# Kernel optimization log

Hardware: AMD Instinct MI355X
Metric: run time of the kernel (lower is better)

## Reference

```python
import jax, jax.numpy as jnp
import numpy as np

BN_EPS = 1e-3  # O-CNN default bn_eps
N_NODES = 150000
C_IN, C_OUT, K = 32, 64, 27  # 3x3x3 octree stencil


def setup_inputs() -> dict:
    key = jax.random.key(0)
    k1, k2, k3 = jax.random.split(key, 3)
    data_in = jax.random.normal(k1, (1, C_IN, N_NODES, 1), dtype=jnp.float32)
    # neighbor table: index == N_NODES marks an empty (zero) neighbor
    neigh = jax.random.randint(k2, (N_NODES, K), 0, N_NODES + 1, dtype=jnp.int32)
    W = jax.random.normal(k3, (C_OUT, C_IN, K), dtype=jnp.float32) * 0.05
    gamma = jnp.ones((C_OUT,), dtype=jnp.float32)
    beta = jnp.zeros((C_OUT,), dtype=jnp.float32)
    return {"data_in": data_in, "neigh": neigh, "W": W, "gamma": gamma, "beta": beta}


def reference(data_in, neigh, W, gamma, beta):
    # data_in: [1, C_in, N, 1] (O-CNN octree feature layout)
    x = data_in[0, :, :, 0]                                  # [C_in, N]
    # pad one zero column so neighbor index == N gathers zeros (empty octant)
    x_pad = jnp.concatenate([x, jnp.zeros((x.shape[0], 1), x.dtype)], axis=1)
    g = x_pad[:, neigh]                                      # [C_in, N, K] im2col gather
    y = jnp.einsum('oik,ink->on', W, g)                      # [C_out, N] GEMM
    # BatchNorm2d (training mode): stats per channel over all nodes, biased var
    mean = jnp.mean(y, axis=1, keepdims=True)
    var = jnp.mean(jnp.square(y - mean), axis=1, keepdims=True)
    yn = (y - mean) * jax.lax.rsqrt(var + BN_EPS)
    out = jnp.maximum(yn * gamma[:, None] + beta[:, None], 0.0)  # affine + ReLU
    return out[None, :, :, None]                             # [1, C_out, N, 1]
```

## Files before the change

kernel.cpp:

```cpp
#include <hip/hip_runtime.h>
#include <hip/hip_bf16.h>
#include <stdint.h>

#define N_NODES 150000
#define C_IN 32
#define C_OUT 64
#define K_TAPS 27
#define K_PAD 28
#define PF 3
#define NSTEP 7
#define NSLOTS 32
#define Y_STRIDE 150016

#define TRANS_BLOCKS 2344
#define WPREP_BLOCKS 224
#define CONV_BLOCKS 4688
#define WS_NEED 28934656ull

typedef __attribute__((ext_vector_type(8))) __bf16 bf16x8;
typedef __attribute__((ext_vector_type(4))) float f32x4;
typedef __attribute__((ext_vector_type(4))) uint32_t u32x4;

__device__ __forceinline__ ushort f2bf(float f) {
    union { float f; uint32_t u; } v; v.f = f;
    uint32_t u = v.u;
    return (ushort)((u + 0x7FFFu + ((u >> 16) & 1u)) >> 16);
}

__global__ __launch_bounds__(256) void k_prep(const float* __restrict__ x,
                                              ushort* __restrict__ xT,
                                              const float* __restrict__ W,
                                              ushort* __restrict__ A_frag,
                                              float* __restrict__ stats) {
    int t = threadIdx.x;
    int b = blockIdx.x;
    if (b < TRANS_BLOCKS) {
        __shared__ float tile[32][65];
        int nb = b * 64;
        int nl = t & 63, i4 = t >> 6;
#pragma unroll
        for (int rep = 0; rep < 8; ++rep) {
            int i = rep * 4 + i4;
            int n = nb + nl;
            tile[i][nl] = (n < N_NODES) ? x[(size_t)i * N_NODES + n] : 0.0f;
        }
        __syncthreads();
        int nr = t >> 2, c0 = (t & 3) * 8;
        int n = nb + nr;
        if (n <= N_NODES) {
            uint32_t w[4];
#pragma unroll
            for (int j = 0; j < 4; ++j) {
                ushort lo = f2bf(tile[c0 + 2 * j][nr]);
                ushort hi = f2bf(tile[c0 + 2 * j + 1][nr]);
                w[j] = (uint32_t)lo | ((uint32_t)hi << 16);
            }
            *reinterpret_cast<uint4*>(xT + (size_t)n * 32 + c0) =
                make_uint4(w[0], w[1], w[2], w[3]);
        }
    } else {
        int tid = (b - TRANS_BLOCKS) * 256 + t;
        if (tid < NSLOTS * 128 + 128) stats[tid] = 0.0f;
        if (tid < C_OUT * C_IN * K_PAD) {
            int j = tid & 7;
            int ln = (tid >> 3) & 63;
            int km = tid >> 9;
            int m = km & 3;
            int k = km >> 2;
            int o = m * 16 + (ln & 15);
            int i = (ln >> 4) * 8 + j;
            A_frag[tid] =
                (k < K_TAPS) ? f2bf(W[o * (C_IN * K_TAPS) + i * K_TAPS + k]) : (ushort)0;
        }
    }
}

__global__ __launch_bounds__(256, 4) void k_conv(const ushort* __restrict__ xT,
                                                 const ushort* __restrict__ A_frag,
                                                 const int* __restrict__ neigh,
                                                 float* __restrict__ yf,
                                                 ushort* __restrict__ yb,
                                                 float* __restrict__ stats,
                                                 int use_bf16) {
    __shared__ int soff[32 * K_PAD];
    __shared__ float sacc[C_OUT * 32];
    int t = threadIdx.x;
    int nb = blockIdx.x * 32;
    for (int j = t; j < 32 * K_PAD; j += 256) {
        int n = j / K_PAD;
        int kk = j - n * K_PAD;
        int ng = nb + n;
        int idx = (kk < K_TAPS && ng < N_NODES) ? neigh[(size_t)ng * K_TAPS + kk]
                                                : N_NODES;
        soff[j] = idx << 6;
    }
    __syncthreads();

    int wid = t >> 6, lane = t & 63;
    int l15 = lane & 15, quad = lane >> 4;
    int qoff = quad << 4;

    const char* xTb = (const char*)xT;
    const char* aB = (const char*)A_frag + (size_t)lane * 16;

    f32x4 acc[4][2];
#pragma unroll
    for (int m = 0; m < 4; ++m)
#pragma unroll
        for (int g = 0; g < 2; ++g) acc[m][g] = (f32x4){0.f, 0.f, 0.f, 0.f};

    bf16x8 bb[PF][2], aa[PF][4];
#pragma unroll
    for (int s = 0; s < PF; ++s) {
        int k = wid + 4 * s;
#pragma unroll
        for (int g = 0; g < 2; ++g)
            bb[s][g] = *reinterpret_cast<const bf16x8*>(
                xTb + (uint32_t)soff[(g * 16 + l15) * K_PAD + k] + qoff);
#pragma unroll
        for (int m = 0; m < 4; ++m)
            aa[s][m] = *reinterpret_cast<const bf16x8*>(aB + ((size_t)(k * 4 + m) << 10));
    }

#pragma unroll
    for (int s = 0; s < NSTEP; ++s) {
        int cur = s % PF;
#pragma unroll
        for (int m = 0; m < 4; ++m)
#pragma unroll
            for (int g = 0; g < 2; ++g)
                acc[m][g] = __builtin_amdgcn_mfma_f32_16x16x32_bf16(
                    aa[cur][m], bb[cur][g], acc[m][g], 0, 0, 0);
        if (s < NSTEP - PF) {
            int kn = wid + 4 * (s + PF);
#pragma unroll
            for (int g = 0; g < 2; ++g)
                bb[cur][g] = *reinterpret_cast<const bf16x8*>(
                    xTb + (uint32_t)soff[(g * 16 + l15) * K_PAD + kn] + qoff);
#pragma unroll
            for (int m = 0; m < 4; ++m)
                aa[cur][m] = *reinterpret_cast<const bf16x8*>(
                    aB + ((size_t)(kn * 4 + m) << 10));
        }
    }

    if (wid == 0) {
#pragma unroll
        for (int m = 0; m < 4; ++m)
#pragma unroll
            for (int g = 0; g < 2; ++g)
#pragma unroll
                for (int r = 0; r < 4; ++r)
                    sacc[(m * 16 + quad * 4 + r) * 32 + g * 16 + l15] = acc[m][g][r];
    }
    __syncthreads();
#pragma unroll
    for (int w = 1; w < 4; ++w) {
        if (wid == w) {
#pragma unroll
            for (int m = 0; m < 4; ++m)
#pragma unroll
                for (int g = 0; g < 2; ++g)
#pragma unroll
                    for (int r = 0; r < 4; ++r)
                        sacc[(m * 16 + quad * 4 + r) * 32 + g * 16 + l15] +=
                            acc[m][g][r];
        }
        __syncthreads();
    }

    if (use_bf16) {
        int e0 = t * 8;
        int o = t >> 2;
        int n0 = (t & 3) * 8;
        uint32_t w[4];
#pragma unroll
        for (int j = 0; j < 4; ++j) {
            ushort lo = f2bf(sacc[e0 + 2 * j]);
            ushort hi = f2bf(sacc[e0 + 2 * j + 1]);
            w[j] = (uint32_t)lo | ((uint32_t)hi << 16);
        }
        u32x4 v = {w[0], w[1], w[2], w[3]};
        __builtin_nontemporal_store(
            v, reinterpret_cast<u32x4*>(yb + (size_t)o * Y_STRIDE + nb + n0));
    } else {
#pragma unroll
        for (int rep = 0; rep < 8; ++rep) {
            int idx = rep * 256 + t;
            int o = idx >> 5;
            int n = nb + (idx & 31);
            if (n < N_NODES)
                __builtin_nontemporal_store(sacc[idx], &yf[(size_t)o * N_NODES + n]);
        }
    }

    if (wid == 0) {
        int slot = blockIdx.x & (NSLOTS - 1);
#pragma unroll
        for (int m = 0; m < 4; ++m) {
#pragma unroll
            for (int r = 0; r < 4; ++r) {
                int o = m * 16 + quad * 4 + r;
                float s = 0.f, sq = 0.f;
#pragma unroll
                for (int g = 0; g < 2; ++g) {
                    float v = sacc[o * 32 + g * 16 + l15];
                    s += v;
                    sq += v * v;
                }
#pragma unroll
                for (int d = 1; d < 16; d <<= 1) {
                    s += __shfl_xor(s, d);
                    sq += __shfl_xor(sq, d);
                }
                if (l15 == 0) {
                    atomicAdd(&stats[slot * 128 + o], s);
                    atomicAdd(&stats[slot * 128 + 64 + o], sq);
                }
            }
        }
    }
}

__global__ __launch_bounds__(256) void k_bn_relu(const ushort* __restrict__ yb,
                                                 float* __restrict__ out,
                                                 const float* __restrict__ stats,
                                                 const float* __restrict__ gamma,
                                                 const float* __restrict__ beta,
                                                 int use_bf16) {
    __shared__ float s_sc, s_sh;
    int t = threadIdx.x;
    int o = blockIdx.y;
    if (t < 32) {
        float s = stats[t * 128 + o];
        float sq = stats[t * 128 + 64 + o];
#pragma unroll
        for (int d = 1; d < 32; d <<= 1) {
            s += __shfl_xor(s, d);
            sq += __shfl_xor(sq, d);
        }
        if (t == 0) {
            const float invN = 1.0f / (float)N_NODES;
            float mean = s * invN;
            float var = sq * invN - mean * mean;
            float rstd = rsqrtf(var + 1e-3f);
            float sc = gamma[o] * rstd;
            s_sc = sc;
            s_sh = beta[o] - mean * sc;
        }
    }
    __syncthreads();
    float sc = s_sc, sh = s_sh;
    if (use_bf16) {
        const u32x4* row = reinterpret_cast<const u32x4*>(yb + (size_t)o * Y_STRIDE);
        f32x4* orow = reinterpret_cast<f32x4*>(out + (size_t)o * N_NODES);
#pragma unroll
        for (int it = 0; it < 2; ++it) {
            int c = blockIdx.x * 512 + it * 256 + t;
            if (c < N_NODES / 8) {
                u32x4 v = __builtin_nontemporal_load(row + c);
                f32x4 f0, f1;
#pragma unroll
                for (int j = 0; j < 2; ++j) {
                    f0[2 * j] = __uint_as_float(v[j] << 16);
                    f0[2 * j + 1] = __uint_as_float(v[j] & 0xffff0000u);
                    f1[2 * j] = __uint_as_float(v[j + 2] << 16);
                    f1[2 * j + 1] = __uint_as_float(v[j + 2] & 0xffff0000u);
                }
#pragma unroll
                for (int j = 0; j < 4; ++j) {
                    f0[j] = fmaxf(fmaf(f0[j], sc, sh), 0.f);
                    f1[j] = fmaxf(fmaf(f1[j], sc, sh), 0.f);
                }
                __builtin_nontemporal_store(f0, orow + 2 * c);
                __builtin_nontemporal_store(f1, orow + 2 * c + 1);
            }
        }
    } else {
        float4* row = reinterpret_cast<float4*>(out + (size_t)o * N_NODES);
        int base = blockIdx.x * 1024 + t;
#pragma unroll
        for (int it = 0; it < 4; ++it) {
            int i = base + it * 256;
            if (i < N_NODES / 4) {
                float4 v = row[i];
                v.x = fmaxf(fmaf(v.x, sc, sh), 0.f);
                v.y = fmaxf(fmaf(v.y, sc, sh), 0.f);
                v.z = fmaxf(fmaf(v.z, sc, sh), 0.f);
                v.w = fmaxf(fmaf(v.w, sc, sh), 0.f);
                row[i] = v;
            }
        }
    }
}

extern "C" void kernel_launch(void* const* d_in, const int* in_sizes, int n_in,
                              void* d_out, int out_size, void* d_ws, size_t ws_size,
                              hipStream_t stream) {
    const float* data_in = (const float*)d_in[0];
    const int* neigh = (const int*)d_in[1];
    const float* W = (const float*)d_in[2];
    const float* gamma = (const float*)d_in[3];
    const float* beta = (const float*)d_in[4];
    float* out = (float*)d_out;

    char* ws = (char*)d_ws;
    ushort* xT = (ushort*)ws;
    ushort* A_frag = (ushort*)(ws + 9601024);
    float* stats = (float*)(ws + 9715712);
    ushort* yb = (ushort*)(ws + 9732608);

    int use_bf16 = (ws_size >= WS_NEED) ? 1 : 0;

    k_prep<<<TRANS_BLOCKS + WPREP_BLOCKS, 256, 0, stream>>>(data_in, xT, W, A_frag,
                                                            stats);
    k_conv<<<CONV_BLOCKS, 256, 0, stream>>>(xT, A_frag, neigh, out, yb, stats,
                                            use_bf16);
    k_bn_relu<<<dim3(37, C_OUT), 256, 0, stream>>>(yb, out, stats, gamma, beta,
                                                   use_bf16);
}
```

Before: 171.6 us.

## Fuse conv and BN+ReLU into one persistent kernel with a grid barrier

Replaces the separate conv and BN/ReLU kernels with one persistent kernel of 1024 blocks. Each block loops over node tiles doing the gather-GEMM and accumulating per-channel statistics, then waits at a software grid barrier (an atomic counter that k_prep zeroes). After the barrier every block reduces the stats and applies the BN affine plus ReLU in a grid-stride pass. This removes one kernel launch and the gap between the two stages. In exchange it adds a spin-wait barrier, serialises tiles within each block, and relies on all 1024 blocks being resident at once to avoid deadlock.

```diff
diff --git a/kernel.cpp b/kernel.cpp
--- a/kernel.cpp
+++ b/kernel.cpp
@@ -14,7 +14,10 @@
 
 #define TRANS_BLOCKS 2344
 #define WPREP_BLOCKS 224
-#define CONV_BLOCKS 4688
+#define N_TILES 4688
+#define FUSED_BLOCKS 1024
+#define CHUNKS_PER_ROW 18750
+#define TOTAL_CHUNKS (C_OUT * CHUNKS_PER_ROW)
 #define WS_NEED 28934656ull
 
 typedef __attribute__((ext_vector_type(8))) __bf16 bf16x8;
@@ -75,221 +78,225 @@
     }
 }
 
-__global__ __launch_bounds__(256, 4) void k_conv(const ushort* __restrict__ xT,
-                                                 const ushort* __restrict__ A_frag,
-                                                 const int* __restrict__ neigh,
-                                                 float* __restrict__ yf,
-                                                 ushort* __restrict__ yb,
-                                                 float* __restrict__ stats,
-                                                 int use_bf16) {
+__global__ __launch_bounds__(256, 4) void k_fused(
+    const ushort* __restrict__ xT, const ushort* __restrict__ A_frag,
+    const int* __restrict__ neigh, float* __restrict__ out,
+    ushort* __restrict__ yb, float* __restrict__ stats, int* __restrict__ barrier_ctr,
+    const float* __restrict__ gamma, const float* __restrict__ beta, int use_bf16) {
     __shared__ int soff[32 * K_PAD];
     __shared__ float sacc[C_OUT * 32];
+    __shared__ float s_sc[C_OUT], s_sh[C_OUT];
     int t = threadIdx.x;
-    int nb = blockIdx.x * 32;
-    for (int j = t; j < 32 * K_PAD; j += 256) {
-        int n = j / K_PAD;
-        int kk = j - n * K_PAD;
-        int ng = nb + n;
-        int idx = (kk < K_TAPS && ng < N_NODES) ? neigh[(size_t)ng * K_TAPS + kk]
-                                                : N_NODES;
-        soff[j] = idx << 6;
-    }
-    __syncthreads();
-
     int wid = t >> 6, lane = t & 63;
     int l15 = lane & 15, quad = lane >> 4;
     int qoff = quad << 4;
-
     const char* xTb = (const char*)xT;
     const char* aB = (const char*)A_frag + (size_t)lane * 16;
 
-    f32x4 acc[4][2];
-#pragma unroll
-    for (int m = 0; m < 4; ++m)
-#pragma unroll
-        for (int g = 0; g < 2; ++g) acc[m][g] = (f32x4){0.f, 0.f, 0.f, 0.f};
-
-    bf16x8 bb[PF][2], aa[PF][4];
-#pragma unroll
-    for (int s = 0; s < PF; ++s) {
-        int k = wid + 4 * s;
-#pragma unroll
-        for (int g = 0; g < 2; ++g)
-            bb[s][g] = *reinterpret_cast<const bf16x8*>(
-                xTb + (uint32_t)soff[(g * 16 + l15) * K_PAD + k] + qoff);
+    for (int tile = blockIdx.x; tile < N_TILES; tile += FUSED_BLOCKS) {
+        int nb = tile * 32;
+        __syncthreads();
+        for (int j = t; j < 32 * K_PAD; j += 256) {
+            int n = j / K_PAD;
+            int kk = j - n * K_PAD;
+            int ng = nb + n;
+            int idx = (kk < K_TAPS && ng < N_NODES) ? neigh[(size_t)ng * K_TAPS + kk]
+                                                    : N_NODES;
+            soff[j] = idx << 6;
+        }
+        __syncthreads();
+
+        f32x4 acc[4][2];
 #pragma unroll
         for (int m = 0; m < 4; ++m)
-            aa[s][m] = *reinterpret_cast<const bf16x8*>(aB + ((size_t)(k * 4 + m) << 10));
-    }
-
-#pragma unroll
-    for (int s = 0; s < NSTEP; ++s) {
-        int cur = s % PF;
-#pragma unroll
-        for (int m = 0; m < 4; ++m)
+#pragma unroll
+            for (int g = 0; g < 2; ++g) acc[m][g] = (f32x4){0.f, 0.f, 0.f, 0.f};
+
+        bf16x8 bb[PF][2], aa[PF][4];
+#pragma unroll
+        for (int s = 0; s < PF; ++s) {
+            int k = wid + 4 * s;
 #pragma unroll
             for (int g = 0; g < 2; ++g)
-                acc[m][g] = __builtin_amdgcn_mfma_f32_16x16x32_bf16(
-                    aa[cur][m], bb[cur][g], acc[m][g], 0, 0, 0);
-        if (s < NSTEP - PF) {
-            int kn = wid + 4 * (s + PF);
-#pragma unroll
-            for (int g = 0; g < 2; ++g)
-                bb[cur][g] = *reinterpret_cast<const bf16x8*>(
-                    xTb + (uint32_t)soff[(g * 16 + l15) * K_PAD + kn] + qoff);
+                bb[s][g] = *reinterpret_cast<const bf16x8*>(
+                    xTb + (uint32_t)soff[(g * 16 + l15) * K_PAD + k] + qoff);
 #pragma unroll
             for (int m = 0; m < 4; ++m)
-                aa[cur][m] = *reinterpret_cast<const bf16x8*>(
-                    aB + ((size_t)(kn * 4 + m) << 10));
-        }
-    }
-
-    if (wid == 0) {
-#pragma unroll
-        for (int m = 0; m < 4; ++m)
-#pragma unroll
-            for (int g = 0; g < 2; ++g)
-#pragma unroll
-                for (int r = 0; r < 4; ++r)
-                    sacc[(m * 16 + quad * 4 + r) * 32 + g * 16 + l15] = acc[m][g][r];
-    }
+                aa[s][m] =
+                    *reinterpret_cast<const bf16x8*>(aB + ((size_t)(k * 4 + m) << 10));
+        }
+
+#pragma unroll
+        for (int s = 0; s < NSTEP; ++s) {
+            int cur = s % PF;
+#pragma unroll
+            for (int m = 0; m < 4; ++m)
+#pragma unroll
+                for (int g = 0; g < 2; ++g)
+                    acc[m][g] = __builtin_amdgcn_mfma_f32_16x16x32_bf16(
+                        aa[cur][m], bb[cur][g], acc[m][g], 0, 0, 0);
+            if (s < NSTEP - PF) {
+                int kn = wid + 4 * (s + PF);
+#pragma unroll
+                for (int g = 0; g < 2; ++g)
+                    bb[cur][g] = *reinterpret_cast<const bf16x8*>(
+                        xTb + (uint32_t)soff[(g * 16 + l15) * K_PAD + kn] + qoff);
+#pragma unroll
+                for (int m = 0; m < 4; ++m)
+                    aa[cur][m] = *reinterpret_cast<const bf16x8*>(
+                        aB + ((size_t)(kn * 4 + m) << 10));
+            }
+        }
+
+        if (wid == 0) {
+#pragma unroll
+            for (int m = 0; m < 4; ++m)
+#pragma unroll
+                for (int g = 0; g < 2; ++g)
+#pragma unroll
+                    for (int r = 0; r < 4; ++r)
+                        sacc[(m * 16 + quad * 4 + r) * 32 + g * 16 + l15] =
+                            acc[m][g][r];
+        }
+        __syncthreads();
+#pragma unroll
+        for (int w = 1; w < 4; ++w) {
+            if (wid == w) {
+#pragma unroll
+                for (int m = 0; m < 4; ++m)
+#pragma unroll
+                    for (int g = 0; g < 2; ++g)
+#pragma unroll
+                        for (int r = 0; r < 4; ++r)
+                            sacc[(m * 16 + quad * 4 + r) * 32 + g * 16 + l15] +=
+                                acc[m][g][r];
+            }
+            __syncthreads();
+        }
+
+        if (use_bf16) {
+            int e0 = t * 8;
+            int o = t >> 2;
+            int n0 = (t & 3) * 8;
+            uint32_t w[4];
+#pragma unroll
+            for (int j = 0; j < 4; ++j) {
+                ushort lo = f2bf(sacc[e0 + 2 * j]);
+                ushort hi = f2bf(sacc[e0 + 2 * j + 1]);
+                w[j] = (uint32_t)lo | ((uint32_t)hi << 16);
+            }
+            u32x4 v = {w[0], w[1], w[2], w[3]};
+            __builtin_nontemporal_store(
+                v, reinterpret_cast<u32x4*>(yb + (size_t)o * Y_STRIDE + nb + n0));
+        } else {
+#pragma unroll
+            for (int rep = 0; rep < 8; ++rep) {
+                int idx = rep * 256 + t;
+                int o = idx >> 5;
+                int n = nb + (idx & 31);
+                if (n < N_NODES)
+                    __builtin_nontemporal_store(sacc[idx],
+                                                &out[(size_t)o * N_NODES + n]);
+            }
+        }
+
+        if (wid == 0) {
+            int slot = tile & (NSLOTS - 1);
+#pragma unroll
+            for (int m = 0; m < 4; ++m) {
+#pragma unroll
+                for (int r = 0; r < 4; ++r) {
+                    int o = m * 16 + quad * 4 + r;
+                    float s = 0.f, sq = 0.f;
+#pragma unroll
+                    for (int g = 0; g < 2; ++g) {
+                        float v = sacc[o * 32 + g * 16 + l15];
+                        s += v;
+                        sq += v * v;
+                    }
+#pragma unroll
+                    for (int d = 1; d < 16; d <<= 1) {
+                        s += __shfl_xor(s, d);
+                        sq += __shfl_xor(sq, d);
+                    }
+                    if (l15 == 0) {
+                        atomicAdd(&stats[slot * 128 + o], s);
+                        atomicAdd(&stats[slot * 128 + 64 + o], sq);
+                    }
+                }
+            }
+        }
+    }
+
+    __threadfence();
     __syncthreads();
-#pragma unroll
-    for (int w = 1; w < 4; ++w) {
-        if (wid == w) {
-#pragma unroll
-            for (int m = 0; m < 4; ++m)
-#pragma unroll
-                for (int g = 0; g < 2; ++g)
-#pragma unroll
-                    for (int r = 0; r < 4; ++r)
-                        sacc[(m * 16 + quad * 4 + r) * 32 + g * 16 + l15] +=
-                            acc[m][g][r];
-        }
-        __syncthreads();
-    }
+    if (t == 0) {
+        __hip_atomic_fetch_add(barrier_ctr, 1, __ATOMIC_ACQ_REL,
+                               __HIP_MEMORY_SCOPE_AGENT);
+        while (__hip_atomic_load(barrier_ctr, __ATOMIC_ACQUIRE,
+                                 __HIP_MEMORY_SCOPE_AGENT) < FUSED_BLOCKS) {
+            __builtin_amdgcn_s_sleep(8);
+        }
+    }
+    __syncthreads();
+    __threadfence();
+
+    if (t < C_OUT) {
+        float s = 0.f, sq = 0.f;
+        for (int c = 0; c < NSLOTS; ++c) {
+            s += __hip_atomic_load(&stats[c * 128 + t], __ATOMIC_RELAXED,
+                                   __HIP_MEMORY_SCOPE_AGENT);
+            sq += __hip_atomic_load(&stats[c * 128 + 64 + t], __ATOMIC_RELAXED,
+                                    __HIP_MEMORY_SCOPE_AGENT);
+        }
+        const float invN = 1.0f / (float)N_NODES;
+        float mean = s * invN;
+        float var = sq * invN - mean * mean;
+        float rstd = rsqrtf(var + 1e-3f);
+        float sc = gamma[t] * rstd;
+        s_sc[t] = sc;
+        s_sh[t] = beta[t] - mean * sc;
+    }
+    __syncthreads();
 
     if (use_bf16) {
-        int e0 = t * 8;
-        int o = t >> 2;
-        int n0 = (t & 3) * 8;
-        uint32_t w[4];
-#pragma unroll
-        for (int j = 0; j < 4; ++j) {
-            ushort lo = f2bf(sacc[e0 + 2 * j]);
-            ushort hi = f2bf(sacc[e0 + 2 * j + 1]);
-            w[j] = (uint32_t)lo | ((uint32_t)hi << 16);
-        }
-        u32x4 v = {w[0], w[1], w[2], w[3]};
-        __builtin_nontemporal_store(
-            v, reinterpret_cast<u32x4*>(yb + (size_t)o * Y_STRIDE + nb + n0));
+        for (int c = blockIdx.x * 256 + t; c < TOTAL_CHUNKS; c += FUSED_BLOCKS * 256) {
+            int o = c / CHUNKS_PER_ROW;
+            int pos = (c - o * CHUNKS_PER_ROW) * 8;
+            float sc = s_sc[o], sh = s_sh[o];
+            u32x4 v = __builtin_nontemporal_load(
+                reinterpret_cast<const u32x4*>(yb + (size_t)o * Y_STRIDE + pos));
+            f32x4 f0, f1;
+#pragma unroll
+            for (int j = 0; j < 2; ++j) {
+                f0[2 * j] = __uint_as_float(v[j] << 16);
+                f0[2 * j + 1] = __uint_as_float(v[j] & 0xffff0000u);
+                f1[2 * j] = __uint_as_float(v[j + 2] << 16);
+                f1[2 * j + 1] = __uint_as_float(v[j + 2] & 0xffff0000u);
+            }
+#pragma unroll
+            for (int j = 0; j < 4; ++j) {
+                f0[j] = fmaxf(fmaf(f0[j], sc, sh), 0.f);
+                f1[j] = fmaxf(fmaf(f1[j], sc, sh), 0.f);
+            }
+            f32x4* op = reinterpret_cast<f32x4*>(out + (size_t)o * N_NODES + pos);
+            __builtin_nontemporal_store(f0, op);
+            __builtin_nontemporal_store(f1, op + 1);
+        }
     } else {
-#pragma unroll
-        for (int rep = 0; rep < 8; ++rep) {
-            int idx = rep * 256 + t;
-            int o = idx >> 5;
-            int n = nb + (idx & 31);
-            if (n < N_NODES)
-                __builtin_nontemporal_store(sacc[idx], &yf[(size_t)o * N_NODES + n]);
-        }
-    }
-
-    if (wid == 0) {
-        int slot = blockIdx.x & (NSLOTS - 1);
-#pragma unroll
-        for (int m = 0; m < 4; ++m) {
-#pragma unroll
-            for (int r = 0; r < 4; ++r) {
-                int o = m * 16 + quad * 4 + r;
-                float s = 0.f, sq = 0.f;
-#pragma unroll
-                for (int g = 0; g < 2; ++g) {
-                    float v = sacc[o * 32 + g * 16 + l15];
-                    s += v;
-                    sq += v * v;
-                }
-#pragma unroll
-                for (int d = 1; d < 16; d <<= 1) {
-                    s += __shfl_xor(s, d);
-                    sq += __shfl_xor(sq, d);
-                }
-                if (l15 == 0) {
-                    atomicAdd(&stats[slot * 128 + o], s);
-                    atomicAdd(&stats[slot * 128 + 64 + o], sq);
-                }
-            }
-        }
-    }
-}
-
-__global__ __launch_bounds__(256) void k_bn_relu(const ushort* __restrict__ yb,
-                                                 float* __restrict__ out,
-                                                 const float* __restrict__ stats,
-                                                 const float* __restrict__ gamma,
-                                                 const float* __restrict__ beta,
-                                                 int use_bf16) {
-    __shared__ float s_sc, s_sh;
-    int t = threadIdx.x;
-    int o = blockIdx.y;
-    if (t < 32) {
-        float s = stats[t * 128 + o];
-        float sq = stats[t * 128 + 64 + o];
-#pragma unroll
-        for (int d = 1; d < 32; d <<= 1) {
-            s += __shfl_xor(s, d);
-            sq += __shfl_xor(sq, d);
-        }
-        if (t == 0) {
-            const float invN = 1.0f / (float)N_NODES;
-            float mean = s * invN;
-            float var = sq * invN - mean * mean;
-            float rstd = rsqrtf(var + 1e-3f);
-            float sc = gamma[o] * rstd;
-            s_sc = sc;
-            s_sh = beta[o] - mean * sc;
-        }
-    }
-    __syncthreads();
-    float sc = s_sc, sh = s_sh;
-    if (use_bf16) {
-        const u32x4* row = reinterpret_cast<const u32x4*>(yb + (size_t)o * Y_STRIDE);
-        f32x4* orow = reinterpret_cast<f32x4*>(out + (size_t)o * N_NODES);
-#pragma unroll
-        for (int it = 0; it < 2; ++it) {
-            int c = blockIdx.x * 512 + it * 256 + t;
-            if (c < N_NODES / 8) {
-                u32x4 v = __builtin_nontemporal_load(row + c);
-                f32x4 f0, f1;
-#pragma unroll
-                for (int j = 0; j < 2; ++j) {
-                    f0[2 * j] = __uint_as_float(v[j] << 16);
-                    f0[2 * j + 1] = __uint_as_float(v[j] & 0xffff0000u);
-                    f1[2 * j] = __uint_as_float(v[j + 2] << 16);
-                    f1[2 * j + 1] = __uint_as_float(v[j + 2] & 0xffff0000u);
-                }
-#pragma unroll
-                for (int j = 0; j < 4; ++j) {
-                    f0[j] = fmaxf(fmaf(f0[j], sc, sh), 0.f);
-                    f1[j] = fmaxf(fmaf(f1[j], sc, sh), 0.f);
-                }
-                __builtin_nontemporal_store(f0, orow + 2 * c);
-                __builtin_nontemporal_store(f1, orow + 2 * c + 1);
-            }
-        }
-    } else {
-        float4* row = reinterpret_cast<float4*>(out + (size_t)o * N_NODES);
-        int base = blockIdx.x * 1024 + t;
-#pragma unroll
-        for (int it = 0; it < 4; ++it) {
-            int i = base + it * 256;
-            if (i < N_NODES / 4) {
-                float4 v = row[i];
-                v.x = fmaxf(fmaf(v.x, sc, sh), 0.f);
-                v.y = fmaxf(fmaf(v.y, sc, sh), 0.f);
-                v.z = fmaxf(fmaf(v.z, sc, sh), 0.f);
-                v.w = fmaxf(fmaf(v.w, sc, sh), 0.f);
-                row[i] = v;
-            }
+        for (int c = blockIdx.x * 256 + t; c < TOTAL_CHUNKS; c += FUSED_BLOCKS * 256) {
+            int o = c / CHUNKS_PER_ROW;
+            int pos = (c - o * CHUNKS_PER_ROW) * 8;
+            float sc = s_sc[o], sh = s_sh[o];
+            f32x4* op = reinterpret_cast<f32x4*>(out + (size_t)o * N_NODES + pos);
+            f32x4 f0 = op[0], f1 = op[1];
+#pragma unroll
+            for (int j = 0; j < 4; ++j) {
+                f0[j] = fmaxf(fmaf(f0[j], sc, sh), 0.f);
+                f1[j] = fmaxf(fmaf(f1[j], sc, sh), 0.f);
+            }
+            op[0] = f0;
+            op[1] = f1;
         }
     }
 }
@@ -308,14 +315,13 @@
     ushort* xT = (ushort*)ws;
     ushort* A_frag = (ushort*)(ws + 9601024);
     float* stats = (float*)(ws + 9715712);
+    int* barrier_ctr = (int*)(ws + 9715712 + NSLOTS * 128 * 4);
     ushort* yb = (ushort*)(ws + 9732608);
 
     int use_bf16 = (ws_size >= WS_NEED) ? 1 : 0;
 
     k_prep<<<TRANS_BLOCKS + WPREP_BLOCKS, 256, 0, stream>>>(data_in, xT, W, A_frag,
                                                             stats);
-    k_conv<<<CONV_BLOCKS, 256, 0, stream>>>(xT, A_frag, neigh, out, yb, stats,
-                                            use_bf16);
-    k_bn_relu<<<dim3(37, C_OUT), 256, 0, stream>>>(yb, out, stats, gamma, beta,
-                                                   use_bf16);
+    k_fused<<<FUSED_BLOCKS, 256, 0, stream>>>(xT, A_frag, neigh, out, yb, stats,
+                                              barrier_ctr, gamma, beta, use_bf16);
 }
```

After: 664.3 us. 3.87x slower.
